# Kernel optimization log

Hardware: AMD Instinct MI355X
Metric: run time of the kernel (lower is better)

Reference implementation:

```python
import jax, jax.numpy as jnp
import numpy as np

B, S, H = 1, 2048, 2048
NH = 16
HS = H // NH  # 128
NEG = -65504.0  # fp16 min used as additive mask value


def setup_inputs() -> dict:
    key = jax.random.key(0)
    k1, k2, k3, k4, k5 = jax.random.split(key, 5)
    hidden_states = jax.random.normal(k1, (B, S, H), dtype=jnp.float32)
    # causal left-to-right mask: 1 where attention allowed
    ltor_mask = jnp.tril(jnp.ones((S, S), dtype=jnp.float32))[None, None, :, :]
    W_qkv = jax.random.normal(k2, (H, 3 * H), dtype=jnp.float32) * (1.0 / np.sqrt(H))
    b_qkv = jax.random.normal(k3, (3 * H,), dtype=jnp.float32) * 0.01
    W_dense = jax.random.normal(k4, (H, H), dtype=jnp.float32) * (1.0 / np.sqrt(H))
    b_dense = jax.random.normal(k5, (H,), dtype=jnp.float32) * 0.01
    return {"hidden_states": hidden_states, "ltor_mask": ltor_mask,
            "W_qkv": W_qkv, "b_qkv": b_qkv, "W_dense": W_dense, "b_dense": b_dense}


def reference(hidden_states, ltor_mask, W_qkv, b_qkv, W_dense, b_dense):
    b, s, h = hidden_states.shape
    # fused QKV projection, then split along last dim (matches split_tensor_along_last_dim)
    qkv = hidden_states @ W_qkv + b_qkv  # [b, s, 3h]
    q, k, v = jnp.split(qkv, 3, axis=-1)
    q = q.reshape(b, s, NH, HS)
    k = k.reshape(b, s, NH, HS)
    v = v.reshape(b, s, NH, HS)
    scale = 1.0 / np.sqrt(HS)  # softmax_scale=None -> 1/sqrt(headdim)
    scores = jnp.einsum('bqhd,bkhd->bhqk', q, k) * scale
    scores = scores + NEG * (1.0 - ltor_mask)  # additive mask, [b,1,s,s] broadcast over heads
    probs = jax.nn.softmax(scores, axis=-1)
    ctx = jnp.einsum('bhqk,bkhd->bqhd', probs, v).reshape(b, s, h)
    out = ctx @ W_dense + b_dense  # output_dropout is identity in eval
    return out
```

## Files before the change

### kernel.cpp

```cpp
#include <hip/hip_runtime.h>
#include <math.h>

#define S_LEN 2048
#define HDIM  2048
#define NHEAD 16
#define HSZ   128
#define H3    6144

typedef __attribute__((ext_vector_type(8))) short bf16x8;
typedef __attribute__((ext_vector_type(4))) float f32x4;

__device__ inline ushort f2bf(float f) {
    union { float f; unsigned u; } c; c.f = f;
    unsigned u = c.u;
    return (ushort)((u + 0x7fffu + ((u >> 16) & 1u)) >> 16);
}
__device__ inline ushort f2bf_trunc(float f) {
    union { float f; unsigned u; } c; c.f = f;
    return (ushort)(c.u >> 16);
}

__global__ __launch_bounds__(256) void cvt_bf16(const float* __restrict__ in,
                                                ushort* __restrict__ out, int n) {
    int i = (blockIdx.x * 256 + threadIdx.x) * 4;
    if (i >= n) return;
    float4 v = *(const float4*)(in + i);
    ushort4 o;
    o.x = f2bf(v.x); o.y = f2bf(v.y); o.z = f2bf(v.z); o.w = f2bf(v.w);
    *(ushort4*)(out + i) = o;
}

__global__ __launch_bounds__(256) void transpose_cvt(const float* __restrict__ W,
                                                     ushort* __restrict__ Wt,
                                                     int K, int N) {
    __shared__ ushort t[64][66];
    const int n0 = blockIdx.x * 64, k0 = blockIdx.y * 64;
    const int tx = threadIdx.x & 15;
    const int ty = threadIdx.x >> 4;
    #pragma unroll
    for (int p = 0; p < 4; p++) {
        const int k = p * 16 + ty;
        float4 v = *(const float4*)(&W[(size_t)(k0 + k) * N + n0 + tx * 4]);
        t[k][tx * 4 + 0] = f2bf(v.x);
        t[k][tx * 4 + 1] = f2bf(v.y);
        t[k][tx * 4 + 2] = f2bf(v.z);
        t[k][tx * 4 + 3] = f2bf(v.w);
    }
    __syncthreads();
    #pragma unroll
    for (int p = 0; p < 4; p++) {
        const int n = p * 16 + ty;
        ushort4 o;
        o.x = t[tx * 4 + 0][n];
        o.y = t[tx * 4 + 1][n];
        o.z = t[tx * 4 + 2][n];
        o.w = t[tx * 4 + 3][n];
        *(ushort4*)(&Wt[(size_t)(n0 + n) * K + k0 + tx * 4]) = o;
    }
}

__global__ __launch_bounds__(256) void transpose_v(const ushort* __restrict__ qkvb,
                                                   ushort* __restrict__ Vtb) {
    __shared__ ushort t[64][66];
    const int s0 = blockIdx.x * 64;
    const int d0 = blockIdx.y * 64;
    const int tx = threadIdx.x & 15;
    const int ty = threadIdx.x >> 4;
    #pragma unroll
    for (int p = 0; p < 4; p++) {
        const int s = p * 16 + ty;
        ushort4 v = *(const ushort4*)(&qkvb[(size_t)(s0 + s) * H3 + 2 * HDIM + d0 + tx * 4]);
        *(ushort4*)(&t[s][tx * 4]) = v;
    }
    __syncthreads();
    #pragma unroll
    for (int p = 0; p < 4; p++) {
        const int d = p * 16 + ty;
        ushort4 o;
        o.x = t[tx * 4 + 0][d];
        o.y = t[tx * 4 + 1][d];
        o.z = t[tx * 4 + 2][d];
        o.w = t[tx * 4 + 3][d];
        *(ushort4*)(&Vtb[(size_t)(d0 + d) * S_LEN + s0 + tx * 4]) = o;
    }
}

template <bool BF16_OUT>
__global__ __launch_bounds__(256) void gemm_bt_bias(
    const ushort* __restrict__ A, const ushort* __restrict__ Bt,
    const float* __restrict__ bias, float* __restrict__ C,
    ushort* __restrict__ Cb, int M, int N, int K)
{
    __shared__ ushort sA[128 * 32];
    __shared__ ushort sB[128 * 32];

    const int tid  = threadIdx.x;
    const int m0   = blockIdx.y * 128;
    const int n0   = blockIdx.x * 128;
    const int w    = tid >> 6;
    const int lane = tid & 63;
    const int quad = lane >> 4;
    const int l16  = lane & 15;
    const int wr   = (w >> 1) * 64;
    const int wc   = (w & 1) * 64;

    f32x4 acc[4][4] = {};

    const int row_l = tid >> 2;
    const int kc_l  = (tid & 3) * 8;

    for (int k0 = 0; k0 < K; k0 += 32) {
        #pragma unroll
        for (int iss = 0; iss < 2; iss++) {
            const int li  = iss * 256 + tid;
            const int row = iss * 64 + row_l;
            const ushort* ga = A  + (size_t)(m0 + row) * K + k0 + kc_l;
            const ushort* gb = Bt + (size_t)(n0 + row) * K + k0 + kc_l;
            __builtin_amdgcn_global_load_lds(
                (const __attribute__((address_space(1))) void*)ga,
                (__attribute__((address_space(3))) void*)(sA + li * 8), 16, 0, 0);
            __builtin_amdgcn_global_load_lds(
                (const __attribute__((address_space(1))) void*)gb,
                (__attribute__((address_space(3))) void*)(sB + li * 8), 16, 0, 0);
        }
        __syncthreads();

        bf16x8 af[4], bq[4];
        #pragma unroll
        for (int i = 0; i < 4; i++)
            af[i] = *(const bf16x8*)(sA + (wr + i * 16 + l16) * 32 + quad * 8);
        #pragma unroll
        for (int j = 0; j < 4; j++)
            bq[j] = *(const bf16x8*)(sB + (wc + j * 16 + l16) * 32 + quad * 8);

        #pragma unroll
        for (int i = 0; i < 4; i++)
            #pragma unroll
            for (int j = 0; j < 4; j++)
                acc[i][j] = __builtin_amdgcn_mfma_f32_16x16x32_bf16(
                    af[i], bq[j], acc[i][j], 0, 0, 0);
        __syncthreads();
    }

    #pragma unroll
    for (int i = 0; i < 4; i++) {
        #pragma unroll
        for (int r = 0; r < 4; r++) {
            const int m = m0 + wr + i * 16 + quad * 4 + r;
            #pragma unroll
            for (int j = 0; j < 4; j++) {
                const int n = n0 + wc + j * 16 + l16;
                float v = acc[i][j][r] + bias[n];
                if (BF16_OUT) {
                    float vp = __shfl_xor(v, 1, 64);
                    unsigned both = (unsigned)f2bf(v) | ((unsigned)f2bf(vp) << 16);
                    if ((l16 & 1) == 0)
                        *(unsigned*)(Cb + (size_t)m * N + n) = both;
                } else {
                    C[(size_t)m * N + n] = v;
                }
            }
        }
    }
}

__global__ __launch_bounds__(256) void attn_mfma(
    const ushort* __restrict__ qkvb, const ushort* __restrict__ Vtb,
    ushort* __restrict__ ctxb)
{
    __shared__ __align__(16) ushort sK [2][64 * 128];
    __shared__ __align__(16) ushort sVt[2][128 * 64];
    __shared__ __align__(16) ushort Ps [4 * 1024];

    const int tid  = threadIdx.x;
    const int bid  = blockIdx.x;
    const int h    = bid & 15;
    const int qt   = (bid < 256) ? (31 - (bid >> 4)) : ((bid - 256) >> 4);
    const int q0   = qt * 64;
    const int w    = tid >> 6;
    const int lane = tid & 63;
    const int quad = lane >> 4;
    const int l16  = lane & 15;
    const int qr0  = q0 + w * 16;

    const float scale = 0.08838834764831845f;

    bf16x8 qf[4];
    #pragma unroll
    for (int c = 0; c < 4; c++)
        qf[c] = *(const bf16x8*)(qkvb + (size_t)(qr0 + l16) * H3 + h * HSZ + c * 32 + quad * 8);

    f32x4 o[8] = {};
    float lsum[4] = {0.f, 0.f, 0.f, 0.f};

    const int nt   = qt + 1;
    const int skey = tid >> 2;
    const int sq8  = tid & 3;

    auto stage = [&](int kt, int b) {
        const int k0 = kt * 64;
        #pragma unroll
        for (int iss = 0; iss < 4; iss++) {
            const int li = iss * 256 + tid;
            const ushort* g = qkvb + (size_t)(k0 + skey) * H3 + HDIM + h * HSZ + iss * 32 + sq8 * 8;
            __builtin_amdgcn_global_load_lds(
                (const __attribute__((address_space(1))) void*)g,
                (__attribute__((address_space(3))) void*)(&sK[b][0] + li * 8), 16, 0, 0);
        }
        #pragma unroll
        for (int iss = 0; iss < 4; iss++) {
            const int li = iss * 256 + tid;
            const int c  = li >> 9;
            const int d  = (li >> 2) & 127;
            const ushort* g = Vtb + (size_t)(h * HSZ + d) * S_LEN + k0 + c * 32 + (li & 3) * 8;
            __builtin_amdgcn_global_load_lds(
                (const __attribute__((address_space(1))) void*)g,
                (__attribute__((address_space(3))) void*)(&sVt[b][0] + li * 8), 16, 0, 0);
        }
    };

    stage(0, 0);

    const int wofs = w * 1024;

    for (int kt = 0; kt < nt; kt++) {
        const int b  = kt & 1;
        const int k0 = kt * 64;

        if (kt + 1 < nt) {
            stage(kt + 1, b ^ 1);
            asm volatile("s_waitcnt vmcnt(8)" ::: "memory");
        } else {
            asm volatile("s_waitcnt vmcnt(0)" ::: "memory");
        }
        asm volatile("s_barrier" ::: "memory");

        const ushort* bK = &sK[b][0];
        const ushort* bV = &sVt[b][0];

        f32x4 sacc[4] = {};
        #pragma unroll
        for (int jt = 0; jt < 4; jt++)
            #pragma unroll
            for (int c = 0; c < 4; c++) {
                bf16x8 kf = *(const bf16x8*)(bK + c * 2048 + (jt * 16 + l16) * 32 + quad * 8);
                sacc[jt] = __builtin_amdgcn_mfma_f32_16x16x32_bf16(qf[c], kf, sacc[jt], 0, 0, 0);
            }

        float p[4][4];
        if (kt == nt - 1) {
            #pragma unroll
            for (int jt = 0; jt < 4; jt++) {
                const int key = k0 + jt * 16 + l16;
                #pragma unroll
                for (int r = 0; r < 4; r++) {
                    float e = __expf(sacc[jt][r] * scale);
                    if (key > qr0 + quad * 4 + r) e = 0.f;
                    p[jt][r] = e;
                    lsum[r] += e;
                }
            }
        } else {
            #pragma unroll
            for (int jt = 0; jt < 4; jt++)
                #pragma unroll
                for (int r = 0; r < 4; r++) {
                    float e = __expf(sacc[jt][r] * scale);
                    p[jt][r] = e;
                    lsum[r] += e;
                }
        }

        #pragma unroll
        for (int jt = 0; jt < 4; jt++) {
            const int cpan = jt >> 1;
            const int lch  = (jt & 1) * 2 + (l16 >> 3);
            const int phys = lch ^ quad;
            #pragma unroll
            for (int r = 0; r < 4; r++) {
                const int row = quad * 4 + r;
                Ps[wofs + cpan * 512 + row * 32 + phys * 8 + (l16 & 7)] = f2bf_trunc(p[jt][r]);
            }
        }

        #pragma unroll
        for (int c = 0; c < 2; c++) {
            const int pph = quad ^ (l16 >> 2);
            bf16x8 pf = *(const bf16x8*)(Ps + wofs + c * 512 + l16 * 32 + pph * 8);
            #pragma unroll
            for (int ht = 0; ht < 8; ht++) {
                bf16x8 vf = *(const bf16x8*)(bV + c * 4096 + (ht * 16 + l16) * 32 + quad * 8);
                o[ht] = __builtin_amdgcn_mfma_f32_16x16x32_bf16(pf, vf, o[ht], 0, 0, 0);
            }
        }

        asm volatile("s_waitcnt lgkmcnt(0)" ::: "memory");
        asm volatile("s_barrier" ::: "memory");
    }

    float invl[4];
    #pragma unroll
    for (int r = 0; r < 4; r++) {
        float ls = lsum[r];
        #pragma unroll
        for (int off = 1; off < 16; off <<= 1)
            ls += __shfl_xor(ls, off, 64);
        invl[r] = 1.0f / ls;
    }
    #pragma unroll
    for (int ht = 0; ht < 8; ht++) {
        #pragma unroll
        for (int r = 0; r < 4; r++) {
            float v  = o[ht][r] * invl[r];
            float vp = __shfl_xor(v, 1, 64);
            unsigned both = (unsigned)f2bf(v) | ((unsigned)f2bf(vp) << 16);
            if ((l16 & 1) == 0)
                *(unsigned*)(ctxb + (size_t)(qr0 + quad * 4 + r) * HDIM + h * HSZ + ht * 16 + l16) = both;
        }
    }
}

extern "C" void kernel_launch(void* const* d_in, const int* in_sizes, int n_in,
                              void* d_out, int out_size, void* d_ws, size_t ws_size,
                              hipStream_t stream) {
    const float* X    = (const float*)d_in[0];
    const float* Wqkv = (const float*)d_in[2];
    const float* bqkv = (const float*)d_in[3];
    const float* Wd   = (const float*)d_in[4];
    const float* bd   = (const float*)d_in[5];
    float* out = (float*)d_out;

    ushort* Xb   = (ushort*)d_ws;
    ushort* Wqt  = Xb   + (size_t)S_LEN * HDIM;
    ushort* Wdt  = Wqt  + (size_t)H3 * HDIM;
    ushort* ctxb = Wdt  + (size_t)HDIM * HDIM;
    ushort* qkvb = ctxb + (size_t)S_LEN * HDIM;
    ushort* Vtb  = qkvb + (size_t)S_LEN * H3;

    dim3 blk(256);

    cvt_bf16<<<dim3((S_LEN * HDIM) / 1024), blk, 0, stream>>>(X, Xb, S_LEN * HDIM);
    transpose_cvt<<<dim3(H3 / 64, HDIM / 64), blk, 0, stream>>>(Wqkv, Wqt, HDIM, H3);
    transpose_cvt<<<dim3(HDIM / 64, HDIM / 64), blk, 0, stream>>>(Wd, Wdt, HDIM, HDIM);

    gemm_bt_bias<true><<<dim3(H3 / 128, S_LEN / 128), blk, 0, stream>>>(
        Xb, Wqt, bqkv, nullptr, qkvb, S_LEN, H3, HDIM);

    transpose_v<<<dim3(S_LEN / 64, HDIM / 64), blk, 0, stream>>>(qkvb, Vtb);

    attn_mfma<<<dim3(512), blk, 0, stream>>>(qkvb, Vtb, ctxb);

    gemm_bt_bias<false><<<dim3(HDIM / 128, S_LEN / 128), blk, 0, stream>>>(
        ctxb, Wdt, bd, out, nullptr, S_LEN, HDIM, HDIM);
}
```

Measured before the change: 314.3 us.

## Merge prep kernels, fuse V transpose into QKV GEMM, double-buffer GEMMs

Folds the three conversion and transpose launches into a single prep kernel. The QKV GEMM now writes the V slice directly in transposed layout, which removes the separate transpose_v pass. Both GEMMs gain double-buffered LDS staging with manual waitcnt and barriers so global loads overlap the MFMA work. The dense projection uses 64-row tiles to launch more blocks. Together this cuts launch count and intermediate traffic, at the cost of more LDS per block and hand-tuned wait counts that must match the number of issued loads.

```diff
diff --git a/kernel.cpp b/kernel.cpp
--- a/kernel.cpp
+++ b/kernel.cpp
@@ -20,23 +20,36 @@
     return (ushort)(c.u >> 16);
 }
 
-__global__ __launch_bounds__(256) void cvt_bf16(const float* __restrict__ in,
-                                                ushort* __restrict__ out, int n) {
-    int i = (blockIdx.x * 256 + threadIdx.x) * 4;
-    if (i >= n) return;
-    float4 v = *(const float4*)(in + i);
-    ushort4 o;
-    o.x = f2bf(v.x); o.y = f2bf(v.y); o.z = f2bf(v.z); o.w = f2bf(v.w);
-    *(ushort4*)(out + i) = o;
-}
-
-__global__ __launch_bounds__(256) void transpose_cvt(const float* __restrict__ W,
-                                                     ushort* __restrict__ Wt,
-                                                     int K, int N) {
+__global__ __launch_bounds__(256) void prep(
+    const float* __restrict__ X,    ushort* __restrict__ Xb,
+    const float* __restrict__ Wqkv, ushort* __restrict__ Wqt,
+    const float* __restrict__ Wd,   ushort* __restrict__ Wdt)
+{
     __shared__ ushort t[64][66];
-    const int n0 = blockIdx.x * 64, k0 = blockIdx.y * 64;
-    const int tx = threadIdx.x & 15;
-    const int ty = threadIdx.x >> 4;
+    const int bid = blockIdx.x;
+    const int tid = threadIdx.x;
+
+    if (bid < 4096) {
+        int i = bid * 1024 + tid * 4;
+        float4 v = *(const float4*)(X + i);
+        ushort4 o;
+        o.x = f2bf(v.x); o.y = f2bf(v.y); o.z = f2bf(v.z); o.w = f2bf(v.w);
+        *(ushort4*)(Xb + i) = o;
+        return;
+    }
+
+    const float* W; ushort* Wt; int K, N, n0, k0;
+    if (bid < 7168) {
+        const int b = bid - 4096;
+        W = Wqkv; Wt = Wqt; K = HDIM; N = H3;
+        n0 = (b % 96) * 64; k0 = (b / 96) * 64;
+    } else {
+        const int b = bid - 7168;
+        W = Wd; Wt = Wdt; K = HDIM; N = HDIM;
+        n0 = (b % 32) * 64; k0 = (b / 32) * 64;
+    }
+    const int tx = tid & 15;
+    const int ty = tid >> 4;
     #pragma unroll
     for (int p = 0; p < 4; p++) {
         const int k = p * 16 + ty;
@@ -59,40 +72,13 @@
     }
 }
 
-__global__ __launch_bounds__(256) void transpose_v(const ushort* __restrict__ qkvb,
-                                                   ushort* __restrict__ Vtb) {
-    __shared__ ushort t[64][66];
-    const int s0 = blockIdx.x * 64;
-    const int d0 = blockIdx.y * 64;
-    const int tx = threadIdx.x & 15;
-    const int ty = threadIdx.x >> 4;
-    #pragma unroll
-    for (int p = 0; p < 4; p++) {
-        const int s = p * 16 + ty;
-        ushort4 v = *(const ushort4*)(&qkvb[(size_t)(s0 + s) * H3 + 2 * HDIM + d0 + tx * 4]);
-        *(ushort4*)(&t[s][tx * 4]) = v;
-    }
-    __syncthreads();
-    #pragma unroll
-    for (int p = 0; p < 4; p++) {
-        const int d = p * 16 + ty;
-        ushort4 o;
-        o.x = t[tx * 4 + 0][d];
-        o.y = t[tx * 4 + 1][d];
-        o.z = t[tx * 4 + 2][d];
-        o.w = t[tx * 4 + 3][d];
-        *(ushort4*)(&Vtb[(size_t)(d0 + d) * S_LEN + s0 + tx * 4]) = o;
-    }
-}
-
-template <bool BF16_OUT>
-__global__ __launch_bounds__(256) void gemm_bt_bias(
+__global__ __launch_bounds__(256) void gemm_qkv(
     const ushort* __restrict__ A, const ushort* __restrict__ Bt,
-    const float* __restrict__ bias, float* __restrict__ C,
-    ushort* __restrict__ Cb, int M, int N, int K)
+    const float* __restrict__ bias, ushort* __restrict__ qkvb,
+    ushort* __restrict__ Vtb)
 {
-    __shared__ ushort sA[128 * 32];
-    __shared__ ushort sB[128 * 32];
+    __shared__ ushort sA[2][128 * 32];
+    __shared__ ushort sB[2][128 * 32];
 
     const int tid  = threadIdx.x;
     const int m0   = blockIdx.y * 128;
@@ -106,32 +92,43 @@
 
     f32x4 acc[4][4] = {};
 
-    const int row_l = tid >> 2;
-    const int kc_l  = (tid & 3) * 8;
-
-    for (int k0 = 0; k0 < K; k0 += 32) {
+    auto stage = [&](int k0, int b) {
         #pragma unroll
         for (int iss = 0; iss < 2; iss++) {
             const int li  = iss * 256 + tid;
-            const int row = iss * 64 + row_l;
-            const ushort* ga = A  + (size_t)(m0 + row) * K + k0 + kc_l;
-            const ushort* gb = Bt + (size_t)(n0 + row) * K + k0 + kc_l;
+            const int row = li >> 2;
+            const int kc  = (li & 3) * 8;
+            const ushort* ga = A  + (size_t)(m0 + row) * HDIM + k0 + kc;
+            const ushort* gb = Bt + (size_t)(n0 + row) * HDIM + k0 + kc;
             __builtin_amdgcn_global_load_lds(
                 (const __attribute__((address_space(1))) void*)ga,
-                (__attribute__((address_space(3))) void*)(sA + li * 8), 16, 0, 0);
+                (__attribute__((address_space(3))) void*)(&sA[b][0] + li * 8), 16, 0, 0);
             __builtin_amdgcn_global_load_lds(
                 (const __attribute__((address_space(1))) void*)gb,
-                (__attribute__((address_space(3))) void*)(sB + li * 8), 16, 0, 0);
-        }
-        __syncthreads();
+                (__attribute__((address_space(3))) void*)(&sB[b][0] + li * 8), 16, 0, 0);
+        }
+    };
+
+    stage(0, 0);
+    const int NIT = HDIM / 32;
+
+    for (int kt = 0; kt < NIT; kt++) {
+        const int b = kt & 1;
+        if (kt + 1 < NIT) {
+            stage((kt + 1) * 32, b ^ 1);
+            asm volatile("s_waitcnt vmcnt(4)" ::: "memory");
+        } else {
+            asm volatile("s_waitcnt vmcnt(0)" ::: "memory");
+        }
+        asm volatile("s_barrier" ::: "memory");
 
         bf16x8 af[4], bq[4];
         #pragma unroll
         for (int i = 0; i < 4; i++)
-            af[i] = *(const bf16x8*)(sA + (wr + i * 16 + l16) * 32 + quad * 8);
+            af[i] = *(const bf16x8*)(&sA[b][0] + (wr + i * 16 + l16) * 32 + quad * 8);
         #pragma unroll
         for (int j = 0; j < 4; j++)
-            bq[j] = *(const bf16x8*)(sB + (wc + j * 16 + l16) * 32 + quad * 8);
+            bq[j] = *(const bf16x8*)(&sB[b][0] + (wc + j * 16 + l16) * 32 + quad * 8);
 
         #pragma unroll
         for (int i = 0; i < 4; i++)
@@ -139,26 +136,41 @@
             for (int j = 0; j < 4; j++)
                 acc[i][j] = __builtin_amdgcn_mfma_f32_16x16x32_bf16(
                     af[i], bq[j], acc[i][j], 0, 0, 0);
-        __syncthreads();
-    }
-
-    #pragma unroll
-    for (int i = 0; i < 4; i++) {
-        #pragma unroll
-        for (int r = 0; r < 4; r++) {
-            const int m = m0 + wr + i * 16 + quad * 4 + r;
-            #pragma unroll
-            for (int j = 0; j < 4; j++) {
-                const int n = n0 + wc + j * 16 + l16;
-                float v = acc[i][j][r] + bias[n];
-                if (BF16_OUT) {
+
+        asm volatile("s_waitcnt lgkmcnt(0)" ::: "memory");
+        asm volatile("s_barrier" ::: "memory");
+    }
+
+    if (n0 < 2 * HDIM) {
+        #pragma unroll
+        for (int i = 0; i < 4; i++)
+            #pragma unroll
+            for (int r = 0; r < 4; r++) {
+                const int m = m0 + wr + i * 16 + quad * 4 + r;
+                #pragma unroll
+                for (int j = 0; j < 4; j++) {
+                    const int n = n0 + wc + j * 16 + l16;
+                    float v = acc[i][j][r] + bias[n];
                     float vp = __shfl_xor(v, 1, 64);
                     unsigned both = (unsigned)f2bf(v) | ((unsigned)f2bf(vp) << 16);
                     if ((l16 & 1) == 0)
-                        *(unsigned*)(Cb + (size_t)m * N + n) = both;
-                } else {
-                    C[(size_t)m * N + n] = v;
+                        *(unsigned*)(qkvb + (size_t)m * H3 + n) = both;
                 }
+            }
+    } else {
+        #pragma unroll
+        for (int i = 0; i < 4; i++) {
+            const int mb = m0 + wr + i * 16 + quad * 4;
+            #pragma unroll
+            for (int j = 0; j < 4; j++) {
+                const int n = n0 + wc + j * 16 + l16;
+                const float bv = bias[n];
+                ushort4 o;
+                o.x = f2bf(acc[i][j][0] + bv);
+                o.y = f2bf(acc[i][j][1] + bv);
+                o.z = f2bf(acc[i][j][2] + bv);
+                o.w = f2bf(acc[i][j][3] + bv);
+                *(ushort4*)(&Vtb[(size_t)(n - 2 * HDIM) * S_LEN + mb]) = o;
             }
         }
     }
@@ -220,7 +232,6 @@
     };
 
     stage(0, 0);
-
     const int wofs = w * 1024;
 
     for (int kt = 0; kt < nt; kt++) {
@@ -320,6 +331,91 @@
     }
 }
 
+__global__ __launch_bounds__(256) void gemm_dense(
+    const ushort* __restrict__ A, const ushort* __restrict__ Bt,
+    const float* __restrict__ bias, float* __restrict__ C)
+{
+    __shared__ ushort sA[2][64 * 32];
+    __shared__ ushort sB[2][128 * 32];
+
+    const int tid  = threadIdx.x;
+    const int m0   = blockIdx.y * 64;
+    const int n0   = blockIdx.x * 128;
+    const int w    = tid >> 6;
+    const int lane = tid & 63;
+    const int quad = lane >> 4;
+    const int l16  = lane & 15;
+    const int wr   = (w >> 1) * 32;
+    const int wc   = (w & 1) * 64;
+
+    f32x4 acc[2][4] = {};
+
+    auto stage = [&](int k0, int b) {
+        {
+            const int row = tid >> 2;
+            const int kc  = (tid & 3) * 8;
+            const ushort* ga = A + (size_t)(m0 + row) * HDIM + k0 + kc;
+            __builtin_amdgcn_global_load_lds(
+                (const __attribute__((address_space(1))) void*)ga,
+                (__attribute__((address_space(3))) void*)(&sA[b][0] + tid * 8), 16, 0, 0);
+        }
+        #pragma unroll
+        for (int iss = 0; iss < 2; iss++) {
+            const int li  = iss * 256 + tid;
+            const int row = li >> 2;
+            const int kc  = (li & 3) * 8;
+            const ushort* gb = Bt + (size_t)(n0 + row) * HDIM + k0 + kc;
+            __builtin_amdgcn_global_load_lds(
+                (const __attribute__((address_space(1))) void*)gb,
+                (__attribute__((address_space(3))) void*)(&sB[b][0] + li * 8), 16, 0, 0);
+        }
+    };
+
+    stage(0, 0);
+    const int NIT = HDIM / 32;
+
+    for (int kt = 0; kt < NIT; kt++) {
+        const int b = kt & 1;
+        if (kt + 1 < NIT) {
+            stage((kt + 1) * 32, b ^ 1);
+            asm volatile("s_waitcnt vmcnt(3)" ::: "memory");
+        } else {
+            asm volatile("s_waitcnt vmcnt(0)" ::: "memory");
+        }
+        asm volatile("s_barrier" ::: "memory");
+
+        bf16x8 af[2], bq[4];
+        #pragma unroll
+        for (int i = 0; i < 2; i++)
+            af[i] = *(const bf16x8*)(&sA[b][0] + (wr + i * 16 + l16) * 32 + quad * 8);
+        #pragma unroll
+        for (int j = 0; j < 4; j++)
+            bq[j] = *(const bf16x8*)(&sB[b][0] + (wc + j * 16 + l16) * 32 + quad * 8);
+
+        #pragma unroll
+        for (int i = 0; i < 2; i++)
+            #pragma unroll
+            for (int j = 0; j < 4; j++)
+                acc[i][j] = __builtin_amdgcn_mfma_f32_16x16x32_bf16(
+                    af[i], bq[j], acc[i][j], 0, 0, 0);
+
+        asm volatile("s_waitcnt lgkmcnt(0)" ::: "memory");
+        asm volatile("s_barrier" ::: "memory");
+    }
+
+    #pragma unroll
+    for (int i = 0; i < 2; i++)
+        #pragma unroll
+        for (int r = 0; r < 4; r++) {
+            const int m = m0 + wr + i * 16 + quad * 4 + r;
+            #pragma unroll
+            for (int j = 0; j < 4; j++) {
+                const int n = n0 + wc + j * 16 + l16;
+                C[(size_t)m * HDIM + n] = acc[i][j][r] + bias[n];
+            }
+        }
+}
+
 extern "C" void kernel_launch(void* const* d_in, const int* in_sizes, int n_in,
                               void* d_out, int out_size, void* d_ws, size_t ws_size,
                               hipStream_t stream) {
@@ -339,17 +435,13 @@
 
     dim3 blk(256);
 
-    cvt_bf16<<<dim3((S_LEN * HDIM) / 1024), blk, 0, stream>>>(X, Xb, S_LEN * HDIM);
-    transpose_cvt<<<dim3(H3 / 64, HDIM / 64), blk, 0, stream>>>(Wqkv, Wqt, HDIM, H3);
-    transpose_cvt<<<dim3(HDIM / 64, HDIM / 64), blk, 0, stream>>>(Wd, Wdt, HDIM, HDIM);
-
-    gemm_bt_bias<true><<<dim3(H3 / 128, S_LEN / 128), blk, 0, stream>>>(
-        Xb, Wqt, bqkv, nullptr, qkvb, S_LEN, H3, HDIM);
-
-    transpose_v<<<dim3(S_LEN / 64, HDIM / 64), blk, 0, stream>>>(qkvb, Vtb);
+    prep<<<dim3(8192), blk, 0, stream>>>(X, Xb, Wqkv, Wqt, Wd, Wdt);
+
+    gemm_qkv<<<dim3(H3 / 128, S_LEN / 128), blk, 0, stream>>>(
+        Xb, Wqt, bqkv, qkvb, Vtb);
 
     attn_mfma<<<dim3(512), blk, 0, stream>>>(qkvb, Vtb, ctxb);
 
-    gemm_bt_bias<false><<<dim3(HDIM / 128, S_LEN / 128), blk, 0, stream>>>(
-        ctxb, Wdt, bd, out, nullptr, S_LEN, HDIM, HDIM);
-}
+    gemm_dense<<<dim3(HDIM / 128, S_LEN / 64), blk, 0, stream>>>(
+        ctxb, Wdt, bd, out);
+}
```

Result: slower. 324.4 us (+3.2%).
